# Optimization experiments

Hardware: AMD Instinct MI355X
Metric: run time of the kernel (lower is better)

The kernel has to match this reference:

```python
import math
import jax, jax.numpy as jnp
import numpy as np

B, S, D_MODEL, N_HEADS, D_KV = 1, 2048, 1024, 16, 64
NUM_BUCKETS, MAX_DIST = 32, 128


def _relative_position_bucket(rel_pos, bidirectional=True, num_buckets=32, max_distance=128):
    # rel_pos: int32 [S, S] = memory_pos - query_pos
    buckets = jnp.zeros_like(rel_pos)
    if bidirectional:
        num_buckets //= 2
        buckets = buckets + (rel_pos > 0).astype(jnp.int32) * num_buckets
        rel_pos = jnp.abs(rel_pos)
    else:
        rel_pos = -jnp.minimum(rel_pos, 0)
    max_exact = num_buckets // 2
    is_small = rel_pos < max_exact
    # log-spaced buckets for large distances; clamp arg to avoid log(0)
    rp_f = jnp.maximum(rel_pos, 1).astype(jnp.float32)
    large = max_exact + (
        jnp.log(rp_f / max_exact) / math.log(max_distance / max_exact) * (num_buckets - max_exact)
    ).astype(jnp.int32)
    large = jnp.minimum(large, num_buckets - 1)
    return buckets + jnp.where(is_small, rel_pos, large)


def setup_inputs() -> dict:
    key = jax.random.key(0)
    ks = jax.random.split(key, 6)
    scale = 1.0 / math.sqrt(D_MODEL)
    return {
        "hidden_states": jax.random.normal(ks[0], (B, S, D_MODEL), jnp.float32),
        "wq": jax.random.normal(ks[1], (D_MODEL, D_MODEL), jnp.float32) * scale,
        "wk": jax.random.normal(ks[2], (D_MODEL, D_MODEL), jnp.float32) * scale,
        "wv": jax.random.normal(ks[3], (D_MODEL, D_MODEL), jnp.float32) * scale,
        "wo": jax.random.normal(ks[4], (D_MODEL, D_MODEL), jnp.float32) * scale,
        "rel_bias": jax.random.normal(ks[5], (NUM_BUCKETS, N_HEADS), jnp.float32),
    }


def reference(hidden_states, wq, wk, wv, wo, rel_bias):
    b, s, _ = hidden_states.shape
    # projections (nn.Linear: x @ W.T), split heads -> [b, h, s, dk]
    def shape(x):
        return x.reshape(b, s, N_HEADS, D_KV).transpose(0, 2, 1, 3)

    q = shape(hidden_states @ wq.T)
    k = shape(hidden_states @ wk.T)
    v = shape(hidden_states @ wv.T)

    # T5: no 1/sqrt(d) scaling on scores
    scores = jnp.einsum("bhqd,bhkd->bhqk", q, k)

    # relative position bias: [1, h, s, s]
    rel_pos = jnp.arange(s, dtype=jnp.int32)[None, :] - jnp.arange(s, dtype=jnp.int32)[:, None]
    buckets = _relative_position_bucket(rel_pos, bidirectional=True,
                                        num_buckets=NUM_BUCKETS, max_distance=MAX_DIST)
    position_bias = rel_bias[buckets].transpose(2, 0, 1)[None]  # [1, h, s, s]

    attn = jax.nn.softmax(scores + position_bias, axis=-1)
    out = jnp.einsum("bhqk,bhkd->bhqd", attn, v)
    out = out.transpose(0, 2, 1, 3).reshape(b, s, N_HEADS * D_KV)
    return out @ wo.T
```

## Files before the change

kernel.cpp:

```cpp
#include <hip/hip_runtime.h>
#include <hip/hip_bf16.h>

typedef _Float16 f16;
typedef f16 f16x8 __attribute__((ext_vector_type(8)));
typedef f16 f16x4 __attribute__((ext_vector_type(4)));
typedef __fp16 h16x2 __attribute__((ext_vector_type(2)));
typedef float f32x4 __attribute__((ext_vector_type(4)));

#define MFMA_F16(a, b, c) __builtin_amdgcn_mfma_f32_16x16x32_f16((a), (b), (c), 0, 0, 0)
#define LOG2E 1.44269504f
#define EXP2(x) __builtin_amdgcn_exp2f(x)

__device__ __forceinline__ void ld_lds16(const void* g, void* l) {
  __builtin_amdgcn_global_load_lds((const __attribute__((address_space(1))) void*)g,
                                   (__attribute__((address_space(3))) void*)l, 16, 0, 0);
}

__global__ __launch_bounds__(256) void cast_and_bias(
    const float* __restrict__ hs, const float* __restrict__ wq,
    const float* __restrict__ wk, const float* __restrict__ wv,
    const float* __restrict__ wo, const float* __restrict__ rb,
    f16* __restrict__ hb, f16* __restrict__ wqb, f16* __restrict__ wkb,
    f16* __restrict__ wvb, f16* __restrict__ wob, float* __restrict__ btab) {
  if (blockIdx.x < 6144) {
    int idx = blockIdx.x * 256 + threadIdx.x;
    const float* src;
    f16* dst;
    int j;
    float scale = 1.0f;
    if (idx < 524288) {
      src = hs; dst = hb; j = idx;
    } else {
      int t = idx - 524288;
      int w = t >> 18;
      j = t & 262143;
      src = (w == 0) ? wq : (w == 1) ? wk : (w == 2) ? wv : wo;
      dst = (w == 0) ? wqb : (w == 1) ? wkb : (w == 2) ? wvb : wob;
      if (w == 0) scale = LOG2E;
    }
    float4 v = ((const float4*)src)[j];
    f16x4 o;
    o[0] = (f16)(v.x * scale); o[1] = (f16)(v.y * scale);
    o[2] = (f16)(v.z * scale); o[3] = (f16)(v.w * scale);
    ((f16x4*)dst)[j] = o;
  } else {
    int idx = (blockIdx.x - 6144) * 256 + threadIdx.x;
    int h = idx >> 12;
    int t = idx & 4095;
    int rel = t - 2047;
    int bucket = (rel > 0) ? 16 : 0;
    int a = (rel < 0) ? -rel : rel;
    int lg;
    if (a < 8) {
      lg = a;
    } else {
      int cnt = (a >= 12) + (a >= 16) + (a >= 23) + (a >= 32) + (a >= 46) +
                (a >= 64) + (a >= 91);
      lg = 8 + cnt;
    }
    bucket += lg;
    btab[idx] = rb[bucket * 16 + h] * LOG2E;
  }
}

template <int MR>
__device__ __forceinline__ void gemm_mainloop(const f16* __restrict__ A,
                                              const f16* __restrict__ B,
                                              int brow, int bcol,
                                              f16 (*lA)[MR * 16 * 64],
                                              f16 (*lB)[128 * 64],
                                              f32x4 acc[MR][2]) {
  const int tid = threadIdx.x;
  const int lane = tid & 63;
  const int wn = tid >> 6;
  const int lo = lane & 15;
  const int hi = lane >> 4;
  const int sw = lo & 7;
  const int sr = tid >> 3;
  const int se = (((tid & 7) ^ (sr & 7)) << 3);
  const f16* gA = A + (size_t)(brow + sr) * 1024 + se;
  const f16* gB = B + (size_t)(bcol + sr) * 1024 + se;

#define GSTAGE(bi, k0_)                                                        \
  do {                                                                         \
    ld_lds16(gA + (k0_), lA[bi] + tid * 8);                                    \
    if constexpr (MR == 4)                                                     \
      ld_lds16(gA + (k0_) + 32 * 1024, lA[bi] + tid * 8 + 2048);               \
    ld_lds16(gB + (k0_),             lB[bi] + tid * 8);                        \
    ld_lds16(gB + (k0_) + 32 * 1024, lB[bi] + tid * 8 + 2048);                 \
    ld_lds16(gB + (k0_) + 64 * 1024, lB[bi] + tid * 8 + 4096);                 \
    ld_lds16(gB + (k0_) + 96 * 1024, lB[bi] + tid * 8 + 6144);                 \
  } while (0)

  GSTAGE(0, 0);
  __syncthreads();
  for (int k0 = 0; k0 < 1024; k0 += 64) {
    const int bi = (k0 >> 6) & 1;
    if (k0 < 960) GSTAGE(bi ^ 1, k0 + 64);
    f16x8 af[MR][2], bf[2][2];
#pragma unroll
    for (int m = 0; m < MR; ++m)
#pragma unroll
      for (int ks = 0; ks < 2; ++ks)
        af[m][ks] = *(const f16x8*)(lA[bi] + (m * 16 + lo) * 64 +
                                    (((ks << 2) | hi) ^ sw) * 8);
#pragma unroll
    for (int j = 0; j < 2; ++j)
#pragma unroll
      for (int ks = 0; ks < 2; ++ks)
        bf[j][ks] = *(const f16x8*)(lB[bi] + (wn * 32 + j * 16 + lo) * 64 +
                                    (((ks << 2) | hi) ^ sw) * 8);
    __builtin_amdgcn_s_setprio(1);
#pragma unroll
    for (int m = 0; m < MR; ++m)
#pragma unroll
      for (int j = 0; j < 2; ++j)
#pragma unroll
        for (int ks = 0; ks < 2; ++ks)
          acc[m][j] = MFMA_F16(af[m][ks], bf[j][ks], acc[m][j]);
    __builtin_amdgcn_s_setprio(0);
    __syncthreads();
  }
#undef GSTAGE
}

__global__ __launch_bounds__(256) void gemm_qkv(
    const f16* __restrict__ A, const f16* __restrict__ Wq,
    const f16* __restrict__ Wk, const f16* __restrict__ Wv,
    f16* __restrict__ Qo, f16* __restrict__ Ko, f16* __restrict__ VTo) {
  __shared__ __align__(16) f16 lA[2][64 * 64];
  __shared__ __align__(16) f16 lB[2][128 * 64];
  const int z = blockIdx.z;
  const f16* B = (z == 0) ? Wq : (z == 1) ? Wk : Wv;
  const int brow = blockIdx.x * 64, bcol = blockIdx.y * 128;
  f32x4 acc[4][2];
#pragma unroll
  for (int m = 0; m < 4; ++m)
#pragma unroll
    for (int j = 0; j < 2; ++j) acc[m][j] = f32x4{0.f, 0.f, 0.f, 0.f};
  gemm_mainloop<4>(A, B, brow, bcol, lA, lB, acc);
  const int lane = threadIdx.x & 63, wn = threadIdx.x >> 6;
  const int lo = lane & 15, hi = lane >> 4;
  if (z < 2) {
    f16* C = z ? Ko : Qo;
#pragma unroll
    for (int m = 0; m < 4; ++m)
#pragma unroll
      for (int j = 0; j < 2; ++j) {
        int col = bcol + wn * 32 + j * 16 + lo;
        int row0 = brow + m * 16 + hi * 4;
#pragma unroll
        for (int r = 0; r < 4; ++r)
          C[(size_t)(row0 + r) * 1024 + col] = (f16)acc[m][j][r];
      }
  } else {
#pragma unroll
    for (int m = 0; m < 4; ++m)
#pragma unroll
      for (int j = 0; j < 2; ++j) {
        int col = bcol + wn * 32 + j * 16 + lo;
        int g = m * 4 + hi;
        int w = g & 7;
        int gp = (g & 8) | ((w < 4) ? (2 * w) : (2 * (w - 4) + 1));
        int sp = brow + gp * 4;
        f16x4 v4;
#pragma unroll
        for (int r = 0; r < 4; ++r) v4[r] = (f16)acc[m][j][r];
        *(f16x4*)(VTo + (size_t)col * 2048 + sp) = v4;
      }
  }
}

__global__ __launch_bounds__(256) void gemm_out(const f16* __restrict__ A,
                                                const f16* __restrict__ W,
                                                float* __restrict__ C) {
  __shared__ __align__(16) f16 lA[2][32 * 64];
  __shared__ __align__(16) f16 lB[2][128 * 64];
  const int brow = blockIdx.x * 32, bcol = blockIdx.y * 128;
  f32x4 acc[2][2];
#pragma unroll
  for (int m = 0; m < 2; ++m)
#pragma unroll
    for (int j = 0; j < 2; ++j) acc[m][j] = f32x4{0.f, 0.f, 0.f, 0.f};
  gemm_mainloop<2>(A, W, brow, bcol, lA, lB, acc);
  const int lane = threadIdx.x & 63, wn = threadIdx.x >> 6;
  const int lo = lane & 15, hi = lane >> 4;
#pragma unroll
  for (int m = 0; m < 2; ++m)
#pragma unroll
    for (int j = 0; j < 2; ++j) {
      int col = bcol + wn * 32 + j * 16 + lo;
      int row0 = brow + m * 16 + hi * 4;
#pragma unroll
      for (int r = 0; r < 4; ++r)
        C[(size_t)(row0 + r) * 1024 + col] = acc[m][j][r];
    }
}

__global__ __launch_bounds__(256, 2) void attn_kernel(
    const f16* __restrict__ Q, const f16* __restrict__ K,
    const f16* __restrict__ VT, const float* __restrict__ btab,
    f16* __restrict__ AO) {
  __shared__ __align__(16) f16 lK[2][4096];
  __shared__ __align__(16) f16 lV[2][4096];

  const int h = blockIdx.y;
  const int q0 = blockIdx.x * 64;
  const int tid = threadIdx.x;
  const int wave = tid >> 6, lane = tid & 63;
  const int lo = lane & 15, hi = lane >> 4;
  const int sw = lo & 7;
  const int qlo = q0 + wave * 16;
  const int myq = qlo + lo;

  const f16* Kh = K + h * 64;
  const f16* VTh = VT + (size_t)h * 64 * 2048;
  const float* bt = btab + h * 4096 + 2047 - myq;

  f16x8 qf[2];
#pragma unroll
  for (int kk = 0; kk < 2; ++kk)
    qf[kk] = *(const f16x8*)(Q + (size_t)myq * 1024 + h * 64 + kk * 32 + hi * 8);

  const float bp = btab[h * 4096 + 4094];
  const float bn = btab[h * 4096 + 0];

  const int sc0 = wave * 64 + lane;
  const int sc1 = 256 + sc0;
  const int r0 = sc0 >> 3, e0 = (sc0 & 7) ^ (r0 & 7);
  const int r1 = sc1 >> 3, e1 = (sc1 & 7) ^ (r1 & 7);

#define STAGE(bufi, kv)                                                        \
  do {                                                                         \
    ld_lds16(Kh + (size_t)((kv) + r0) * 1024 + e0 * 8, &lK[bufi][sc0 * 8]);    \
    ld_lds16(Kh + (size_t)((kv) + r1) * 1024 + e1 * 8, &lK[bufi][sc1 * 8]);    \
    ld_lds16(VTh + (size_t)r0 * 2048 + (kv) + e0 * 8, &lV[bufi][sc0 * 8]);     \
    ld_lds16(VTh + (size_t)r1 * 2048 + (kv) + e1 * 8, &lV[bufi][sc1 * 8]);     \
  } while (0)

#define BIAS_LOAD(t_, ST)                                                      \
  {                                                                            \
    const int kb_ = (t_) * 64;                                                 \
    const int rmin_ = kb_ - (qlo + 15);                                        \
    const int rmax_ = kb_ + 63 - qlo;                                          \
    if (rmin_ >= 91 || rmax_ <= -91) {                                         \
      const float bf_ = (rmin_ >= 91) ? bp : bn;                               \
      _Pragma("unroll") for (int i_ = 0; i_ < 16; ++i_) bias##ST[i_] = bf_;    \
    } else {                                                                   \
      _Pragma("unroll") for (int i_ = 0; i_ < 16; ++i_)                        \
        bias##ST[i_] = bt[kb_ + (i_ >> 2) * 16 + hi * 4 + (i_ & 3)];           \
    }                                                                          \
  }

  float m_run = -1e30f, l_run = 0.f;
  f32x4 oacc[4];
#pragma unroll
  for (int d = 0; d < 4; ++d) oacc[d] = f32x4{0.f, 0.f, 0.f, 0.f};

  f16x8 vfA[4][2], vfB[4][2];
  f32x4 saccA[4], saccB[4];
  float biasA[16], biasB[16];

#define TILE_FRONT(t_, CUR, NXT)                                               \
  {                                                                            \
    const int b_ = (t_) & 1;                                                   \
    const f16* lKb_ = lK[b_];                                                  \
    const f16* lVb_ = lV[b_];                                                  \
    f16x8 kf_[4][2];                                                           \
    _Pragma("unroll") for (int m_ = 0; m_ < 4; ++m_)                           \
      _Pragma("unroll") for (int kk_ = 0; kk_ < 2; ++kk_)                      \
        kf_[m_][kk_] = *(const f16x8*)&lKb_[(m_ * 16 + lo) * 64 +              \
                                            (((kk_ << 2) | hi) ^ sw) * 8];     \
    _Pragma("unroll") for (int d_ = 0; d_ < 4; ++d_)                           \
      _Pragma("unroll") for (int kk_ = 0; kk_ < 2; ++kk_)                      \
        vf##CUR[d_][kk_] = *(const f16x8*)&lVb_[(d_ * 16 + lo) * 64 +          \
                                                ((kk_ * 4 + hi) ^ sw) * 8];    \
    if ((t_) < 31) STAGE(1 - b_, (t_) * 64 + 64);                              \
    if ((t_) < 31) BIAS_LOAD((t_) + 1, NXT);                                   \
    __builtin_amdgcn_s_setprio(1);                                             \
    _Pragma("unroll") for (int m_ = 0; m_ < 4; ++m_) {                         \
      sacc##CUR[m_] = f32x4{bias##CUR[m_ * 4 + 0], bias##CUR[m_ * 4 + 1],      \
                            bias##CUR[m_ * 4 + 2], bias##CUR[m_ * 4 + 3]};     \
      _Pragma("unroll") for (int kk_ = 0; kk_ < 2; ++kk_)                      \
        sacc##CUR[m_] = MFMA_F16(kf_[m_][kk_], qf[kk_], sacc##CUR[m_]);        \
    }                                                                          \
    __builtin_amdgcn_s_setprio(0);                                             \
  }

#define SOFTMAX_PV(PRV)                                                        \
  {                                                                            \
    float p_[16];                                                              \
    _Pragma("unroll") for (int i_ = 0; i_ < 16; ++i_)                          \
      p_[i_] = sacc##PRV[i_ >> 2][i_ & 3];                                     \
    float x8_[8];                                                              \
    _Pragma("unroll") for (int i_ = 0; i_ < 8; ++i_)                           \
      x8_[i_] = fmaxf(p_[i_], p_[i_ + 8]);                                     \
    float x4_[4];                                                              \
    _Pragma("unroll") for (int i_ = 0; i_ < 4; ++i_)                           \
      x4_[i_] = fmaxf(x8_[i_], x8_[i_ + 4]);                                   \
    float mxl_ = fmaxf(fmaxf(x4_[0], x4_[1]), fmaxf(x4_[2], x4_[3]));          \
    if (!__all(mxl_ <= m_run + 11.5416f)) {         \
      float mx_ = fmaxf(mxl_, __shfl_xor(mxl_, 16, 64));                       \
      mx_ = fmaxf(mx_, __shfl_xor(mx_, 32, 64));                               \
      float mn_ = fmaxf(m_run, mx_);                                           \
      float sc_ = EXP2(m_run - mn_);                                           \
      l_run *= sc_;                                                            \
      _Pragma("unroll") for (int d_ = 0; d_ < 4; ++d_) oacc[d_] *= sc_;        \
      m_run = mn_;                                                             \
    }                                                                          \
    _Pragma("unroll") for (int i_ = 0; i_ < 16; ++i_)                          \
      p_[i_] = EXP2(p_[i_] - m_run);                                           \
    float s8_[8];                                                              \
    _Pragma("unroll") for (int i_ = 0; i_ < 8; ++i_)                           \
      s8_[i_] = p_[i_] + p_[i_ + 8];                                           \
    float s4_[4];                                                              \
    _Pragma("unroll") for (int i_ = 0; i_ < 4; ++i_)                           \
      s4_[i_] = s8_[i_] + s8_[i_ + 4];                                         \
    l_run += (s4_[0] + s4_[1]) + (s4_[2] + s4_[3]);            \
    f16x8 pf_[2];                                                              \
    _Pragma("unroll") for (int kk_ = 0; kk_ < 2; ++kk_) {                      \
      union {                                                                  \
        h16x2 h2[4];                                                           \
        f16x8 v8;                                                              \
      } u_;                                                                    \
      _Pragma("unroll") for (int j_ = 0; j_ < 4; ++j_)                         \
        u_.h2[j_] = __builtin_amdgcn_cvt_pkrtz(p_[kk_ * 8 + 2 * j_],           \
                                               p_[kk_ * 8 + 2 * j_ + 1]);      \
      pf_[kk_] = u_.v8;                                                        \
    }                                                                          \
    __builtin_amdgcn_s_setprio(1);                                             \
    _Pragma("unroll") for (int d_ = 0; d_ < 4; ++d_)                           \
      _Pragma("unroll") for (int kk_ = 0; kk_ < 2; ++kk_)                      \
        oacc[d_] = MFMA_F16(vf##PRV[d_][kk_], pf_[kk_], oacc[d_]);             \
    __builtin_amdgcn_s_setprio(0);                                             \
  }

  BIAS_LOAD(0, A);
  STAGE(0, 0);
  __syncthreads();

  TILE_FRONT(0, A, B);
  __syncthreads();

  for (int k2 = 0; k2 < 15; ++k2) {
    const int t1 = 2 * k2 + 1;
    TILE_FRONT(t1, B, A);
    SOFTMAX_PV(A);
    __syncthreads();
    TILE_FRONT(t1 + 1, A, B);
    SOFTMAX_PV(B);
    __syncthreads();
  }
  TILE_FRONT(31, B, A);
  SOFTMAX_PV(A);
  SOFTMAX_PV(B);

#undef TILE_FRONT
#undef SOFTMAX_PV
#undef BIAS_LOAD
#undef STAGE

  l_run += __shfl_xor(l_run, 16, 64);
  l_run += __shfl_xor(l_run, 32, 64);
  float inv = 1.f / l_run;
#pragma unroll
  for (int d = 0; d < 4; ++d) {
    f16x4 ov;
#pragma unroll
    for (int r = 0; r < 4; ++r) ov[r] = (f16)(oacc[d][r] * inv);
    *(f16x4*)(AO + (size_t)myq * 1024 + h * 64 + d * 16 + hi * 4) = ov;
  }
}

extern "C" void kernel_launch(void* const* d_in, const int* in_sizes, int n_in,
                              void* d_out, int out_size, void* d_ws, size_t ws_size,
                              hipStream_t stream) {
  const float* hs = (const float*)d_in[0];
  const float* wq = (const float*)d_in[1];
  const float* wk = (const float*)d_in[2];
  const float* wv = (const float*)d_in[3];
  const float* wo = (const float*)d_in[4];
  const float* rb = (const float*)d_in[5];

  char* w = (char*)d_ws;
  f16* hb  = (f16*)w; w += (size_t)2048 * 1024 * 2;
  f16* wqb = (f16*)w; w += (size_t)1024 * 1024 * 2;
  f16* wkb = (f16*)w; w += (size_t)1024 * 1024 * 2;
  f16* wvb = (f16*)w; w += (size_t)1024 * 1024 * 2;
  f16* wob = (f16*)w; w += (size_t)1024 * 1024 * 2;
  f16* Qb  = (f16*)w; w += (size_t)2048 * 1024 * 2;
  f16* Kb  = (f16*)w; w += (size_t)2048 * 1024 * 2;
  f16* VTb = (f16*)w; w += (size_t)2048 * 1024 * 2;
  f16* AOb = (f16*)w; w += (size_t)2048 * 1024 * 2;
  float* btab = (float*)w; w += (size_t)16 * 4096 * 4;

  cast_and_bias<<<6400, 256, 0, stream>>>(hs, wq, wk, wv, wo, rb,
                                          hb, wqb, wkb, wvb, wob, btab);
  gemm_qkv<<<dim3(32, 8, 3), 256, 0, stream>>>(hb, wqb, wkb, wvb, Qb, Kb, VTb);
  attn_kernel<<<dim3(32, 16), 256, 0, stream>>>(Qb, Kb, VTb, btab, AOb);
  gemm_out<<<dim3(64, 8), 256, 0, stream>>>(AOb, wob, (float*)d_out);
}
```

Measured before the change: 78.56 us.

## Triple-buffer K/V LDS staging with partial vmcnt waits and stage bias in LDS

After: 79.17 us. No clear change (+0.8%).

```diff
diff --git a/kernel.cpp b/kernel.cpp
--- a/kernel.cpp
+++ b/kernel.cpp
@@ -201,8 +201,9 @@
     const f16* __restrict__ Q, const f16* __restrict__ K,
     const f16* __restrict__ VT, const float* __restrict__ btab,
     f16* __restrict__ AO) {
-  __shared__ __align__(16) f16 lK[2][4096];
-  __shared__ __align__(16) f16 lV[2][4096];
+  __shared__ __align__(16) f16 lK[3][4096];
+  __shared__ __align__(16) f16 lV[3][4096];
+  __shared__ __align__(16) float biasL[2112];
 
   const int h = blockIdx.y;
   const int q0 = blockIdx.x * 64;
@@ -212,10 +213,10 @@
   const int sw = lo & 7;
   const int qlo = q0 + wave * 16;
   const int myq = qlo + lo;
+  const int bofs = 63 - wave * 16 - lo;
 
   const f16* Kh = K + h * 64;
   const f16* VTh = VT + (size_t)h * 64 * 2048;
-  const float* bt = btab + h * 4096 + 2047 - myq;
 
   f16x8 qf[2];
 #pragma unroll
@@ -224,6 +225,12 @@
 
   const float bp = btab[h * 4096 + 4094];
   const float bn = btab[h * 4096 + 0];
+
+  {
+    const float* bsrc = btab + h * 4096 + 1984 - q0;
+    for (int c = tid; c < 528; c += 256)
+      ld_lds16(bsrc + c * 4, biasL + c * 4);
+  }
 
   const int sc0 = wave * 64 + lane;
   const int sc1 = 256 + sc0;
@@ -248,9 +255,21 @@
       _Pragma("unroll") for (int i_ = 0; i_ < 16; ++i_) bias##ST[i_] = bf_;    \
     } else {                                                                   \
       _Pragma("unroll") for (int i_ = 0; i_ < 16; ++i_)                        \
-        bias##ST[i_] = bt[kb_ + (i_ >> 2) * 16 + hi * 4 + (i_ & 3)];           \
+        bias##ST[i_] =                                                         \
+            biasL[kb_ + (i_ >> 2) * 16 + hi * 4 + (i_ & 3) + bofs];            \
     }                                                                          \
   }
+
+#define ENDSLOT4                                                               \
+  do {                                                                         \
+    asm volatile("s_waitcnt vmcnt(4)" ::: "memory");                           \
+    __builtin_amdgcn_s_barrier();                                              \
+  } while (0)
+#define ENDSLOT0                                                               \
+  do {                                                                         \
+    asm volatile("s_waitcnt vmcnt(0)" ::: "memory");                           \
+    __builtin_amdgcn_s_barrier();                                              \
+  } while (0)
 
   float m_run = -1e30f, l_run = 0.f;
   f32x4 oacc[4];
@@ -261,11 +280,10 @@
   f32x4 saccA[4], saccB[4];
   float biasA[16], biasB[16];
 
-#define TILE_FRONT(t_, CUR, NXT)                                               \
+#define TILE_FRONT(t_, bf_, CUR, NXT)                                          \
   {                                                                            \
-    const int b_ = (t_) & 1;                                                   \
-    const f16* lKb_ = lK[b_];                                                  \
-    const f16* lVb_ = lV[b_];                                                  \
+    const f16* lKb_ = lK[bf_];                                                 \
+    const f16* lVb_ = lV[bf_];                                                 \
     f16x8 kf_[4][2];                                                           \
     _Pragma("unroll") for (int m_ = 0; m_ < 4; ++m_)                           \
       _Pragma("unroll") for (int kk_ = 0; kk_ < 2; ++kk_)                      \
@@ -275,7 +293,7 @@
       _Pragma("unroll") for (int kk_ = 0; kk_ < 2; ++kk_)                      \
         vf##CUR[d_][kk_] = *(const f16x8*)&lVb_[(d_ * 16 + lo) * 64 +          \
                                                 ((kk_ * 4 + hi) ^ sw) * 8];    \
-    if ((t_) < 31) STAGE(1 - b_, (t_) * 64 + 64);                              \
+    if ((t_) < 30) STAGE(((t_) + 2) % 3, (t_) * 64 + 128);                     \
     if ((t_) < 31) BIAS_LOAD((t_) + 1, NXT);                                   \
     __builtin_amdgcn_s_setprio(1);                                             \
     _Pragma("unroll") for (int m_ = 0; m_ < 4; ++m_) {                         \
@@ -335,30 +353,39 @@
     __builtin_amdgcn_s_setprio(0);                                             \
   }
 
+  STAGE(0, 0);
+  STAGE(1, 64);
+  asm volatile("s_waitcnt vmcnt(4)" ::: "memory");
+  __builtin_amdgcn_s_barrier();
+
   BIAS_LOAD(0, A);
-  STAGE(0, 0);
-  __syncthreads();
-
-  TILE_FRONT(0, A, B);
-  __syncthreads();
-
-  for (int k2 = 0; k2 < 15; ++k2) {
-    const int t1 = 2 * k2 + 1;
-    TILE_FRONT(t1, B, A);
-    SOFTMAX_PV(A);
-    __syncthreads();
-    TILE_FRONT(t1 + 1, A, B);
-    SOFTMAX_PV(B);
-    __syncthreads();
-  }
-  TILE_FRONT(31, B, A);
-  SOFTMAX_PV(A);
+  TILE_FRONT(0, 0, A, B);
+  ENDSLOT4;
+
+  for (int g = 0; g < 4; ++g) {
+    const int t = 6 * g;
+    TILE_FRONT(t + 1, 1, B, A); SOFTMAX_PV(A); ENDSLOT4;
+    TILE_FRONT(t + 2, 2, A, B); SOFTMAX_PV(B); ENDSLOT4;
+    TILE_FRONT(t + 3, 0, B, A); SOFTMAX_PV(A); ENDSLOT4;
+    TILE_FRONT(t + 4, 1, A, B); SOFTMAX_PV(B); ENDSLOT4;
+    TILE_FRONT(t + 5, 2, B, A); SOFTMAX_PV(A); ENDSLOT4;
+    TILE_FRONT(t + 6, 0, A, B); SOFTMAX_PV(B); ENDSLOT4;
+  }
+  TILE_FRONT(25, 1, B, A); SOFTMAX_PV(A); ENDSLOT4;
+  TILE_FRONT(26, 2, A, B); SOFTMAX_PV(B); ENDSLOT4;
+  TILE_FRONT(27, 0, B, A); SOFTMAX_PV(A); ENDSLOT4;
+  TILE_FRONT(28, 1, A, B); SOFTMAX_PV(B); ENDSLOT4;
+  TILE_FRONT(29, 2, B, A); SOFTMAX_PV(A); ENDSLOT4;
+  TILE_FRONT(30, 0, A, B); SOFTMAX_PV(B); ENDSLOT0;
+  TILE_FRONT(31, 1, B, A); SOFTMAX_PV(A);
   SOFTMAX_PV(B);
 
 #undef TILE_FRONT
 #undef SOFTMAX_PV
 #undef BIAS_LOAD
 #undef STAGE
+#undef ENDSLOT4
+#undef ENDSLOT0
 
   l_run += __shfl_xor(l_run, 16, 64);
   l_run += __shfl_xor(l_run, 32, 64);
```
